# Kernel optimization log

Measured on AMD Instinct MI355X. Metric: run time of the kernel, lower is better.

Reference implementation:

```python
import jax, jax.numpy as jnp
import numpy as np

D_MODEL = 512
N_HEADS = 8
Q_SEQ_LEN = 1024
KV_SEQ_LEN = 1024
N_MODES = 64
D_HEAD = D_MODEL // N_HEADS

# FEDformer frequency_modes (deterministic/lowest branch): lowest n_modes freqs
Q_MODES = np.arange(min(N_MODES, Q_SEQ_LEN // 2))
KV_MODES = np.arange(min(N_MODES, KV_SEQ_LEN // 2))


def setup_inputs() -> dict:
    key = jax.random.key(0)
    kq, kk, kv, kwr, kwi = jax.random.split(key, 5)
    B = 8
    scale = 1.0 / (D_MODEL * D_MODEL)
    return {
        "query": jax.random.normal(kq, (B, N_HEADS, Q_SEQ_LEN, D_HEAD), jnp.float32),
        "key": jax.random.normal(kk, (B, N_HEADS, KV_SEQ_LEN, D_HEAD), jnp.float32),
        "value": jax.random.normal(kv, (B, N_HEADS, KV_SEQ_LEN, D_HEAD), jnp.float32),
        "weights_re": scale * jax.random.uniform(kwr, (N_HEADS, D_HEAD, D_HEAD, len(Q_MODES)), jnp.float32),
        "weights_im": scale * jax.random.uniform(kwi, (N_HEADS, D_HEAD, D_HEAD, len(Q_MODES)), jnp.float32),
    }


def reference(query, key, value, weights_re, weights_im):
    # value is accepted but unused by the original forward (FEA-f variant).
    B, H, L, D = query.shape
    q_modes = jnp.asarray(Q_MODES)
    kv_modes = jnp.asarray(KV_MODES)

    # [B,H,D,L] -> rfft along time -> gather selected frequency modes
    q_fft = jnp.fft.rfft(jnp.swapaxes(query, -2, -1), axis=-1)   # [B,H,D,L//2+1]
    k_fft = jnp.fft.rfft(jnp.swapaxes(key, -2, -1), axis=-1)     # [B,H,D,Lk//2+1]
    q_fft = jnp.take(q_fft, q_modes, axis=-1)                    # [B,H,D,Mq]
    k_fft = jnp.take(k_fft, kv_modes, axis=-1)                   # [B,H,D,Mk]

    # complex attention in frequency domain (no conjugation, as in torch einsum)
    scores_fft = jnp.einsum('bhdq,bhdk->bhqk', q_fft, k_fft)
    attn_fft = jnp.tanh(scores_fft)
    context_fft = jnp.einsum('bhqk,bhdk->bhdq', attn_fft, k_fft)  # [B,H,D,Mq]

    w = (weights_re + 1j * weights_im).astype(jnp.complex64)      # [H,D,D,Mq]
    context_fft = jnp.einsum('bhiq,hijq->bhjq', context_fft, w)   # [B,H,D,Mq]

    # scatter modes back into full rfft spectrum, then irfft
    out_fft = jnp.zeros((B, H, D, L // 2 + 1), jnp.complex64)
    out_fft = out_fft.at[..., q_modes].set(context_fft)
    d_model = H * D
    context = jnp.fft.irfft(out_fft / d_model / d_model, n=L, axis=-1)  # [B,H,D,L]
    return context
```

## Files before the change

### kernel.cpp

```cpp
#include <hip/hip_runtime.h>
#include <hip/hip_bf16.h>
#include <cmath>

#define BATCH 8
#define NH 8
#define BH 64
#define SEQ 1024
#define DH 64
#define NM 64

#define P_PLANE 4096
#define P_FLOATS (2*8*64*2*4096)
#define PR_OFF   P_FLOATS
#define C1C_OFF  (PR_OFF + 2*64*2*4096)
#define C2_OFF   (C1C_OFF + 64*64*64*2)

__global__ __launch_bounds__(256) void k_dft(const float* __restrict__ q,
                                             const float* __restrict__ k,
                                             float* __restrict__ P) {
  const int bid = blockIdx.x;
  const int bh = bid & 63;
  const int inp = (bid >> 6) & 1;
  const int tq = bid >> 7;
  const float* x = (inp ? k : q) + (size_t)bh * (SEQ * DH);

  __shared__ float se[64 * 68], so[64 * 68];
  const int tid = threadIdx.x;
  const int dg = tid & 7;
  const int par = (tid >> 3) & 1;
  const int pg = (tid >> 4) & 1;
  const int mg = tid >> 5;
  const int d0 = dg * 8;

  const int t0g = tq * 64;
  {
    const float4* srcA = reinterpret_cast<const float4*>(x + (size_t)t0g * DH);
    const float4* srcB = reinterpret_cast<const float4*>(x + (size_t)(t0g + 512) * DH);
#pragma unroll
    for (int i = 0; i < 4; ++i) {
      int idx = tid + i * 256;
      int tt = idx >> 4, d4 = (idx & 15) * 4;
      float4 a = srcA[idx], b = srcB[idx];
      *reinterpret_cast<float4*>(&se[tt * 68 + d4]) =
          make_float4(a.x + b.x, a.y + b.y, a.z + b.z, a.w + b.w);
      *reinterpret_cast<float4*>(&so[tt * 68 + d4]) =
          make_float4(a.x - b.x, a.y - b.y, a.z - b.z, a.w - b.w);
    }
  }
  __syncthreads();

  const float* s = pg ? so : se;

  float accr[4][8] = {{0.f}}, acci[4][8] = {{0.f}};
  float stepc[4], steps[4], wr[4], wi[4];
#pragma unroll
  for (int mi = 0; mi < 4; ++mi) {
    const int m = 2 * (mg * 4 + mi) + pg;
    const int ps = (2 * m) & 1023;
    stepc[mi] = cospif((float)ps * (1.0f / 512.0f));
    steps[mi] = -sinpif((float)ps * (1.0f / 512.0f));
    const int p0 = (m * (t0g + par)) & 1023;
    wr[mi] = cospif((float)p0 * (1.0f / 512.0f));
    wi[mi] = -sinpif((float)p0 * (1.0f / 512.0f));
  }

#pragma unroll 4
  for (int k2 = 0; k2 < 32; ++k2) {
    const int tl = 2 * k2 + par;
    float4 a = *reinterpret_cast<const float4*>(&s[tl * 68 + d0]);
    float4 b = *reinterpret_cast<const float4*>(&s[tl * 68 + d0 + 4]);
    float xv[8] = {a.x, a.y, a.z, a.w, b.x, b.y, b.z, b.w};
#pragma unroll
    for (int mi = 0; mi < 4; ++mi) {
      float cwr = wr[mi], cwi = wi[mi];
#pragma unroll
      for (int di = 0; di < 8; ++di) {
        accr[mi][di] = fmaf(cwr, xv[di], accr[mi][di]);
        acci[mi][di] = fmaf(cwi, xv[di], acci[mi][di]);
      }
      float nr = cwr * stepc[mi] - cwi * steps[mi];
      float ni = cwr * steps[mi] + cwi * stepc[mi];
      wr[mi] = nr; wi[mi] = ni;
    }
  }

#pragma unroll
  for (int mi = 0; mi < 4; ++mi) {
#pragma unroll
    for (int di = 0; di < 8; ++di) {
      accr[mi][di] += __shfl_xor(accr[mi][di], 8, 64);
      acci[mi][di] += __shfl_xor(acci[mi][di], 8, 64);
    }
  }

  if (par == 0) {
    const size_t base = (((size_t)inp * 8 + tq) * 64 + bh) * 2 * P_PLANE;
#pragma unroll
    for (int mi = 0; mi < 4; ++mi) {
      const int m = 2 * (mg * 4 + mi) + pg;
      float* pr = P + base + (size_t)m * 64 + d0;
      float* pi = P + base + P_PLANE + (size_t)m * 64 + d0;
      *reinterpret_cast<float4*>(pr) =
          make_float4(accr[mi][0], accr[mi][1], accr[mi][2], accr[mi][3]);
      *reinterpret_cast<float4*>(pr + 4) =
          make_float4(accr[mi][4], accr[mi][5], accr[mi][6], accr[mi][7]);
      *reinterpret_cast<float4*>(pi) =
          make_float4(acci[mi][0], acci[mi][1], acci[mi][2], acci[mi][3]);
      *reinterpret_cast<float4*>(pi + 4) =
          make_float4(acci[mi][4], acci[mi][5], acci[mi][6], acci[mi][7]);
    }
  }
}

__global__ __launch_bounds__(256) void k_red(const float* __restrict__ P,
                                             float* __restrict__ Pr) {
  const int idx = blockIdx.x * 256 + threadIdx.x;
  const int inp = idx >> 17;
  const int r = idx & 131071;
  const float4* p4 = reinterpret_cast<const float4*>(P);
  const size_t base = ((size_t)inp * 8) * 131072 + r;
  float4 acc = p4[base];
#pragma unroll
  for (int t = 1; t < 8; ++t) {
    float4 v = p4[base + (size_t)t * 131072];
    acc.x += v.x; acc.y += v.y; acc.z += v.z; acc.w += v.w;
  }
  reinterpret_cast<float4*>(Pr)[idx] = acc;
}

__device__ __forceinline__ void ctanh_f(float x, float y, float& rr, float& ri) {
  float a = 2.0f * x, b = 2.0f * y;
  if (fabsf(a) > 20.0f) {
    rr = (a > 0.0f) ? 1.0f : -1.0f;
    ri = 0.0f;
  } else {
    float ea = expf(a), ena = expf(-a);
    float sb, cb;
    sincosf(b, &sb, &cb);
    float den = 0.5f * (ea + ena) + cb;
    rr = 0.5f * (ea - ena) / den;
    ri = sb / den;
  }
}

__global__ __launch_bounds__(256) void k_mid_a(const float* __restrict__ Pr,
                                               float* __restrict__ C1c) {
  __shared__ float Kr[64][68], Ki[64][68];
  __shared__ float Qr[8][68], Qi[8][68];
  __shared__ float Ar[8][68], Ai[8][68];
  __shared__ float C1rs[64][9], C1is[64][9];

  const int tid = threadIdx.x;
  const int bh = blockIdx.x >> 3;
  const int qo = blockIdx.x & 7;

  const float4* kbase = reinterpret_cast<const float4*>(Pr + ((size_t)(64 + bh)) * 8192);
  for (int idx = tid; idx < 1024; idx += 256) {
    int kk = idx >> 4, dd = (idx & 15) * 4;
    float4 vr = kbase[idx];
    float4 vi = kbase[idx + 1024];
    *reinterpret_cast<float4*>(&Kr[kk][dd]) = vr;
    *reinterpret_cast<float4*>(&Ki[kk][dd]) = vi;
  }
  {
    const float4* qbase =
        reinterpret_cast<const float4*>(Pr + (size_t)bh * 8192 + (size_t)qo * 8 * 64);
    if (tid < 128) {
      int qi2 = tid >> 4, dd = (tid & 15) * 4;
      float4 vr = qbase[tid];
      float4 vi = qbase[tid + 1024];
      *reinterpret_cast<float4*>(&Qr[qi2][dd]) = vr;
      *reinterpret_cast<float4*>(&Qi[qi2][dd]) = vi;
    }
  }
  __syncthreads();

  {
    const int q = tid >> 5, k0 = tid & 31;
    float sr[2] = {0.f}, si[2] = {0.f};
    for (int d = 0; d < 64; d += 4) {
      const float4 qr = *reinterpret_cast<const float4*>(&Qr[q][d]);
      const float4 qi = *reinterpret_cast<const float4*>(&Qi[q][d]);
#pragma unroll
      for (int j = 0; j < 2; ++j) {
        const int kk = k0 + 32 * j;
        const float4 kr = *reinterpret_cast<const float4*>(&Kr[kk][d]);
        const float4 ki = *reinterpret_cast<const float4*>(&Ki[kk][d]);
        float s0 = sr[j], s1 = si[j];
        s0 = fmaf(qr.x, kr.x, s0); s0 = fmaf(-qi.x, ki.x, s0);
        s1 = fmaf(qr.x, ki.x, s1); s1 = fmaf(qi.x, kr.x, s1);
        s0 = fmaf(qr.y, kr.y, s0); s0 = fmaf(-qi.y, ki.y, s0);
        s1 = fmaf(qr.y, ki.y, s1); s1 = fmaf(qi.y, kr.y, s1);
        s0 = fmaf(qr.z, kr.z, s0); s0 = fmaf(-qi.z, ki.z, s0);
        s1 = fmaf(qr.z, ki.z, s1); s1 = fmaf(qi.z, kr.z, s1);
        s0 = fmaf(qr.w, kr.w, s0); s0 = fmaf(-qi.w, ki.w, s0);
        s1 = fmaf(qr.w, ki.w, s1); s1 = fmaf(qi.w, kr.w, s1);
        sr[j] = s0; si[j] = s1;
      }
    }
#pragma unroll
    for (int j = 0; j < 2; ++j) {
      float rr, ri;
      ctanh_f(sr[j], si[j], rr, ri);
      Ar[q][k0 + 32 * j] = rr;
      Ai[q][k0 + 32 * j] = ri;
    }
  }
  __syncthreads();

  {
    const int q = tid >> 5, d0 = (tid & 31) * 2;
    float cr[2] = {0.f}, ci[2] = {0.f};
    for (int kk = 0; kk < 64; ++kk) {
      float a_r = Ar[q][kk], a_i = Ai[q][kk];
      const float2 kr = *reinterpret_cast<const float2*>(&Kr[kk][d0]);
      const float2 ki = *reinterpret_cast<const float2*>(&Ki[kk][d0]);
      cr[0] = fmaf(a_r, kr.x, cr[0]); cr[0] = fmaf(-a_i, ki.x, cr[0]);
      ci[0] = fmaf(a_r, ki.x, ci[0]); ci[0] = fmaf(a_i, kr.x, ci[0]);
      cr[1] = fmaf(a_r, kr.y, cr[1]); cr[1] = fmaf(-a_i, ki.y, cr[1]);
      ci[1] = fmaf(a_r, ki.y, ci[1]); ci[1] = fmaf(a_i, kr.y, ci[1]);
    }
    C1rs[d0][q] = cr[0];     C1is[d0][q] = ci[0];
    C1rs[d0 + 1][q] = cr[1]; C1is[d0 + 1][q] = ci[1];
  }
  __syncthreads();

  for (int idx = tid; idx < 512; idx += 256) {
    int i = idx >> 3, ql = idx & 7;
    size_t o = (((size_t)bh * 64 + i) * 64 + qo * 8 + ql) * 2;
    *reinterpret_cast<float2*>(&C1c[o]) = make_float2(C1rs[i][ql], C1is[i][ql]);
  }
}

__global__ __launch_bounds__(64) void k_mid_b(const float* __restrict__ C1c,
                                              const float* __restrict__ wre,
                                              const float* __restrict__ wim,
                                              float* __restrict__ C2) {
  const int bid = blockIdx.x;
  const int j = bid & 63;
  const int h = (bid >> 6) & 7;
  const int bq = bid >> 9;
  const int lane = threadIdx.x;

  const int bh0 = (bq * 2 + 0) * 8 + h;
  const int bh1 = (bq * 2 + 1) * 8 + h;
  const float2* c1a = reinterpret_cast<const float2*>(C1c) + (size_t)bh0 * 4096 + lane;
  const float2* c1b = reinterpret_cast<const float2*>(C1c) + (size_t)bh1 * 4096 + lane;
  const float* wrp = wre + ((size_t)h * 4096 + j) * 64 + lane;
  const float* wip = wim + ((size_t)h * 4096 + j) * 64 + lane;

  float ar0 = 0.f, ai0 = 0.f, ar1 = 0.f, ai1 = 0.f;
#pragma unroll 8
  for (int i = 0; i < 64; ++i) {
    float wr = wrp[(size_t)i * 4096];
    float wi = wip[(size_t)i * 4096];
    float2 ca = c1a[(size_t)i * 64];
    float2 cb = c1b[(size_t)i * 64];
    ar0 = fmaf(ca.x, wr, ar0); ar0 = fmaf(-ca.y, wi, ar0);
    ai0 = fmaf(ca.x, wi, ai0); ai0 = fmaf(ca.y, wr, ai0);
    ar1 = fmaf(cb.x, wr, ar1); ar1 = fmaf(-cb.y, wi, ar1);
    ai1 = fmaf(cb.x, wi, ai1); ai1 = fmaf(cb.y, wr, ai1);
  }
  *reinterpret_cast<float2*>(&C2[(((size_t)bh0 * 64 + j) * 64 + lane) * 2]) = make_float2(ar0, ai0);
  *reinterpret_cast<float2*>(&C2[(((size_t)bh1 * 64 + j) * 64 + lane) * 2]) = make_float2(ar1, ai1);
}

__global__ __launch_bounds__(256) void k_idft(const float* __restrict__ C2,
                                              float* __restrict__ out) {
  __shared__ float Cr[64][68], Ci[64][68];
  const int tid = threadIdx.x;
  const int bh = blockIdx.x >> 3;
  const int tc = blockIdx.x & 7;
  const float s = 1.0f / (512.0f * 512.0f * 1024.0f);

  for (int idx = tid; idx < 4096; idx += 256) {
    int j = idx >> 6, m = idx & 63;
    float f = (m == 0) ? s : 2.0f * s;
    float2 c = *reinterpret_cast<const float2*>(&C2[(((size_t)bh * 64 + j) * 64 + m) * 2]);
    Cr[m][j] = f * c.x;
    Ci[m][j] = f * c.y;
  }
  __syncthreads();

  const int tg = tid & 31, jg = tid >> 5;
  const int tp0 = tc * 64 + tg * 2;
  const int j0 = jg * 8;

  float sc[2], ss[2], wc[2], wsn[2];
#pragma unroll
  for (int kk = 0; kk < 2; ++kk) {
    float ph = (float)((tp0 + kk) & 1023) * (1.0f / 512.0f);
    sc[kk] = cospif(ph);
    ss[kk] = sinpif(ph);
    wc[kk] = 1.0f;
    wsn[kk] = 0.0f;
  }

  float accE[2][8] = {{0.f}}, accO[2][8] = {{0.f}};
#pragma unroll 2
  for (int m = 0; m < 64; ++m) {
    float4 c0 = *reinterpret_cast<const float4*>(&Cr[m][j0]);
    float4 c1 = *reinterpret_cast<const float4*>(&Cr[m][j0 + 4]);
    float4 e0 = *reinterpret_cast<const float4*>(&Ci[m][j0]);
    float4 e1 = *reinterpret_cast<const float4*>(&Ci[m][j0 + 4]);
    float crv[8] = {c0.x, c0.y, c0.z, c0.w, c1.x, c1.y, c1.z, c1.w};
    float civ[8] = {e0.x, e0.y, e0.z, e0.w, e1.x, e1.y, e1.z, e1.w};
    float(*acc)[8] = (m & 1) ? accO : accE;
#pragma unroll
    for (int kk = 0; kk < 2; ++kk) {
      float cw = wc[kk], sw = wsn[kk];
#pragma unroll
      for (int jj = 0; jj < 8; ++jj) {
        acc[kk][jj] = fmaf(crv[jj], cw, acc[kk][jj]);
        acc[kk][jj] = fmaf(-civ[jj], sw, acc[kk][jj]);
      }
      float nr = cw * sc[kk] - sw * ss[kk];
      float ni = cw * ss[kk] + sw * sc[kk];
      wc[kk] = nr; wsn[kk] = ni;
    }
  }

#pragma unroll
  for (int jj = 0; jj < 8; ++jj) {
    float e0v = accE[0][jj], o0v = accO[0][jj];
    float e1v = accE[1][jj], o1v = accO[1][jj];
    float* row = &out[((size_t)bh * 64 + j0 + jj) * 1024];
    *reinterpret_cast<float2*>(&row[tp0])       = make_float2(e0v + o0v, e1v + o1v);
    *reinterpret_cast<float2*>(&row[tp0 + 512]) = make_float2(e0v - o0v, e1v - o1v);
  }
}

extern "C" void kernel_launch(void* const* d_in, const int* in_sizes, int n_in,
                              void* d_out, int out_size, void* d_ws, size_t ws_size,
                              hipStream_t stream) {
  const float* q   = (const float*)d_in[0];
  const float* k   = (const float*)d_in[1];
  const float* wre = (const float*)d_in[3];
  const float* wim = (const float*)d_in[4];
  float* out = (float*)d_out;
  float* ws  = (float*)d_ws;

  float* P   = ws;
  float* Pr  = ws + PR_OFF;
  float* C1c = ws + C1C_OFF;
  float* C2  = ws + C2_OFF;

  k_dft  <<<1024, 256, 0, stream>>>(q, k, P);
  k_red  <<<1024, 256, 0, stream>>>(P, Pr);
  k_mid_a<<<512,  256, 0, stream>>>(Pr, C1c);
  k_mid_b<<<2048,  64, 0, stream>>>(C1c, wre, wim, C2);
  k_idft <<<512,  256, 0, stream>>>(C2, out);
}
```

Before: 166.6 us.

## Rebalance work per thread across mid and inverse-DFT kernels for more parallelism

```diff
diff --git a/kernel.cpp b/kernel.cpp
--- a/kernel.cpp
+++ b/kernel.cpp
@@ -146,13 +146,13 @@
 __global__ __launch_bounds__(256) void k_mid_a(const float* __restrict__ Pr,
                                                float* __restrict__ C1c) {
   __shared__ float Kr[64][68], Ki[64][68];
-  __shared__ float Qr[8][68], Qi[8][68];
-  __shared__ float Ar[8][68], Ai[8][68];
-  __shared__ float C1rs[64][9], C1is[64][9];
+  __shared__ float Qr[4][68], Qi[4][68];
+  __shared__ float Ar[4][68], Ai[4][68];
+  __shared__ float C1rs[64][6], C1is[64][6];
 
   const int tid = threadIdx.x;
-  const int bh = blockIdx.x >> 3;
-  const int qo = blockIdx.x & 7;
+  const int bh = blockIdx.x >> 4;
+  const int qo = blockIdx.x & 15;
 
   const float4* kbase = reinterpret_cast<const float4*>(Pr + ((size_t)(64 + bh)) * 8192);
   for (int idx = tid; idx < 1024; idx += 256) {
@@ -164,8 +164,8 @@
   }
   {
     const float4* qbase =
-        reinterpret_cast<const float4*>(Pr + (size_t)bh * 8192 + (size_t)qo * 8 * 64);
-    if (tid < 128) {
+        reinterpret_cast<const float4*>(Pr + (size_t)bh * 8192 + (size_t)qo * 256);
+    if (tid < 64) {
       int qi2 = tid >> 4, dd = (tid & 15) * 4;
       float4 vr = qbase[tid];
       float4 vi = qbase[tid + 1024];
@@ -176,58 +176,47 @@
   __syncthreads();
 
   {
-    const int q = tid >> 5, k0 = tid & 31;
-    float sr[2] = {0.f}, si[2] = {0.f};
+    const int q = tid >> 6, kk = tid & 63;
+    float s0 = 0.f, s1 = 0.f;
     for (int d = 0; d < 64; d += 4) {
       const float4 qr = *reinterpret_cast<const float4*>(&Qr[q][d]);
       const float4 qi = *reinterpret_cast<const float4*>(&Qi[q][d]);
-#pragma unroll
-      for (int j = 0; j < 2; ++j) {
-        const int kk = k0 + 32 * j;
-        const float4 kr = *reinterpret_cast<const float4*>(&Kr[kk][d]);
-        const float4 ki = *reinterpret_cast<const float4*>(&Ki[kk][d]);
-        float s0 = sr[j], s1 = si[j];
-        s0 = fmaf(qr.x, kr.x, s0); s0 = fmaf(-qi.x, ki.x, s0);
-        s1 = fmaf(qr.x, ki.x, s1); s1 = fmaf(qi.x, kr.x, s1);
-        s0 = fmaf(qr.y, kr.y, s0); s0 = fmaf(-qi.y, ki.y, s0);
-        s1 = fmaf(qr.y, ki.y, s1); s1 = fmaf(qi.y, kr.y, s1);
-        s0 = fmaf(qr.z, kr.z, s0); s0 = fmaf(-qi.z, ki.z, s0);
-        s1 = fmaf(qr.z, ki.z, s1); s1 = fmaf(qi.z, kr.z, s1);
-        s0 = fmaf(qr.w, kr.w, s0); s0 = fmaf(-qi.w, ki.w, s0);
-        s1 = fmaf(qr.w, ki.w, s1); s1 = fmaf(qi.w, kr.w, s1);
-        sr[j] = s0; si[j] = s1;
-      }
-    }
-#pragma unroll
-    for (int j = 0; j < 2; ++j) {
-      float rr, ri;
-      ctanh_f(sr[j], si[j], rr, ri);
-      Ar[q][k0 + 32 * j] = rr;
-      Ai[q][k0 + 32 * j] = ri;
-    }
-  }
-  __syncthreads();
-
-  {
-    const int q = tid >> 5, d0 = (tid & 31) * 2;
-    float cr[2] = {0.f}, ci[2] = {0.f};
+      const float4 kr = *reinterpret_cast<const float4*>(&Kr[kk][d]);
+      const float4 ki = *reinterpret_cast<const float4*>(&Ki[kk][d]);
+      s0 = fmaf(qr.x, kr.x, s0); s0 = fmaf(-qi.x, ki.x, s0);
+      s1 = fmaf(qr.x, ki.x, s1); s1 = fmaf(qi.x, kr.x, s1);
+      s0 = fmaf(qr.y, kr.y, s0); s0 = fmaf(-qi.y, ki.y, s0);
+      s1 = fmaf(qr.y, ki.y, s1); s1 = fmaf(qi.y, kr.y, s1);
+      s0 = fmaf(qr.z, kr.z, s0); s0 = fmaf(-qi.z, ki.z, s0);
+      s1 = fmaf(qr.z, ki.z, s1); s1 = fmaf(qi.z, kr.z, s1);
+      s0 = fmaf(qr.w, kr.w, s0); s0 = fmaf(-qi.w, ki.w, s0);
+      s1 = fmaf(qr.w, ki.w, s1); s1 = fmaf(qi.w, kr.w, s1);
+    }
+    float rr, ri;
+    ctanh_f(s0, s1, rr, ri);
+    Ar[q][kk] = rr;
+    Ai[q][kk] = ri;
+  }
+  __syncthreads();
+
+  {
+    const int q = tid >> 6, dd = tid & 63;
+    float cr = 0.f, ci = 0.f;
+#pragma unroll 8
     for (int kk = 0; kk < 64; ++kk) {
       float a_r = Ar[q][kk], a_i = Ai[q][kk];
-      const float2 kr = *reinterpret_cast<const float2*>(&Kr[kk][d0]);
-      const float2 ki = *reinterpret_cast<const float2*>(&Ki[kk][d0]);
-      cr[0] = fmaf(a_r, kr.x, cr[0]); cr[0] = fmaf(-a_i, ki.x, cr[0]);
-      ci[0] = fmaf(a_r, ki.x, ci[0]); ci[0] = fmaf(a_i, kr.x, ci[0]);
-      cr[1] = fmaf(a_r, kr.y, cr[1]); cr[1] = fmaf(-a_i, ki.y, cr[1]);
-      ci[1] = fmaf(a_r, ki.y, ci[1]); ci[1] = fmaf(a_i, kr.y, ci[1]);
-    }
-    C1rs[d0][q] = cr[0];     C1is[d0][q] = ci[0];
-    C1rs[d0 + 1][q] = cr[1]; C1is[d0 + 1][q] = ci[1];
-  }
-  __syncthreads();
-
-  for (int idx = tid; idx < 512; idx += 256) {
-    int i = idx >> 3, ql = idx & 7;
-    size_t o = (((size_t)bh * 64 + i) * 64 + qo * 8 + ql) * 2;
+      float krv = Kr[kk][dd], kiv = Ki[kk][dd];
+      cr = fmaf(a_r, krv, cr); cr = fmaf(-a_i, kiv, cr);
+      ci = fmaf(a_r, kiv, ci); ci = fmaf(a_i, krv, ci);
+    }
+    C1rs[dd][q] = cr;
+    C1is[dd][q] = ci;
+  }
+  __syncthreads();
+
+  {
+    const int i = tid >> 2, ql = tid & 3;
+    size_t o = (((size_t)bh * 64 + i) * 64 + qo * 4 + ql) * 2;
     *reinterpret_cast<float2*>(&C1c[o]) = make_float2(C1rs[i][ql], C1is[i][ql]);
   }
 }
@@ -239,30 +228,25 @@
   const int bid = blockIdx.x;
   const int j = bid & 63;
   const int h = (bid >> 6) & 7;
-  const int bq = bid >> 9;
+  const int b = bid >> 9;
   const int lane = threadIdx.x;
 
-  const int bh0 = (bq * 2 + 0) * 8 + h;
-  const int bh1 = (bq * 2 + 1) * 8 + h;
-  const float2* c1a = reinterpret_cast<const float2*>(C1c) + (size_t)bh0 * 4096 + lane;
-  const float2* c1b = reinterpret_cast<const float2*>(C1c) + (size_t)bh1 * 4096 + lane;
+  const int bh = b * 8 + h;
+  const float2* c1 = reinterpret_cast<const float2*>(C1c) + (size_t)bh * 4096 + lane;
   const float* wrp = wre + ((size_t)h * 4096 + j) * 64 + lane;
   const float* wip = wim + ((size_t)h * 4096 + j) * 64 + lane;
 
-  float ar0 = 0.f, ai0 = 0.f, ar1 = 0.f, ai1 = 0.f;
+  float ar = 0.f, ai = 0.f;
 #pragma unroll 8
   for (int i = 0; i < 64; ++i) {
     float wr = wrp[(size_t)i * 4096];
     float wi = wip[(size_t)i * 4096];
-    float2 ca = c1a[(size_t)i * 64];
-    float2 cb = c1b[(size_t)i * 64];
-    ar0 = fmaf(ca.x, wr, ar0); ar0 = fmaf(-ca.y, wi, ar0);
-    ai0 = fmaf(ca.x, wi, ai0); ai0 = fmaf(ca.y, wr, ai0);
-    ar1 = fmaf(cb.x, wr, ar1); ar1 = fmaf(-cb.y, wi, ar1);
-    ai1 = fmaf(cb.x, wi, ai1); ai1 = fmaf(cb.y, wr, ai1);
-  }
-  *reinterpret_cast<float2*>(&C2[(((size_t)bh0 * 64 + j) * 64 + lane) * 2]) = make_float2(ar0, ai0);
-  *reinterpret_cast<float2*>(&C2[(((size_t)bh1 * 64 + j) * 64 + lane) * 2]) = make_float2(ar1, ai1);
+    float2 c = c1[(size_t)i * 64];
+    ar = fmaf(c.x, wr, ar); ar = fmaf(-c.y, wi, ar);
+    ai = fmaf(c.x, wi, ai); ai = fmaf(c.y, wr, ai);
+  }
+  *reinterpret_cast<float2*>(&C2[(((size_t)bh * 64 + j) * 64 + lane) * 2]) =
+      make_float2(ar, ai);
 }
 
 __global__ __launch_bounds__(256) void k_idft(const float* __restrict__ C2,
@@ -282,13 +266,13 @@
   }
   __syncthreads();
 
-  const int tg = tid & 31, jg = tid >> 5;
-  const int tp0 = tc * 64 + tg * 2;
-  const int j0 = jg * 8;
-
-  float sc[2], ss[2], wc[2], wsn[2];
-#pragma unroll
-  for (int kk = 0; kk < 2; ++kk) {
+  const int tg = tid & 15, jg = tid >> 4;
+  const int tp0 = tc * 64 + tg * 4;
+  const int j0 = jg * 4;
+
+  float sc[4], ss[4], wc[4], wsn[4];
+#pragma unroll
+  for (int kk = 0; kk < 4; ++kk) {
     float ph = (float)((tp0 + kk) & 1023) * (1.0f / 512.0f);
     sc[kk] = cospif(ph);
     ss[kk] = sinpif(ph);
@@ -296,21 +280,19 @@
     wsn[kk] = 0.0f;
   }
 
-  float accE[2][8] = {{0.f}}, accO[2][8] = {{0.f}};
+  float accE[4][4] = {{0.f}}, accO[4][4] = {{0.f}};
 #pragma unroll 2
   for (int m = 0; m < 64; ++m) {
     float4 c0 = *reinterpret_cast<const float4*>(&Cr[m][j0]);
-    float4 c1 = *reinterpret_cast<const float4*>(&Cr[m][j0 + 4]);
     float4 e0 = *reinterpret_cast<const float4*>(&Ci[m][j0]);
-    float4 e1 = *reinterpret_cast<const float4*>(&Ci[m][j0 + 4]);
-    float crv[8] = {c0.x, c0.y, c0.z, c0.w, c1.x, c1.y, c1.z, c1.w};
-    float civ[8] = {e0.x, e0.y, e0.z, e0.w, e1.x, e1.y, e1.z, e1.w};
-    float(*acc)[8] = (m & 1) ? accO : accE;
-#pragma unroll
-    for (int kk = 0; kk < 2; ++kk) {
+    float crv[4] = {c0.x, c0.y, c0.z, c0.w};
+    float civ[4] = {e0.x, e0.y, e0.z, e0.w};
+    float(*acc)[4] = (m & 1) ? accO : accE;
+#pragma unroll
+    for (int kk = 0; kk < 4; ++kk) {
       float cw = wc[kk], sw = wsn[kk];
 #pragma unroll
-      for (int jj = 0; jj < 8; ++jj) {
+      for (int jj = 0; jj < 4; ++jj) {
         acc[kk][jj] = fmaf(crv[jj], cw, acc[kk][jj]);
         acc[kk][jj] = fmaf(-civ[jj], sw, acc[kk][jj]);
       }
@@ -321,12 +303,14 @@
   }
 
 #pragma unroll
-  for (int jj = 0; jj < 8; ++jj) {
-    float e0v = accE[0][jj], o0v = accO[0][jj];
-    float e1v = accE[1][jj], o1v = accO[1][jj];
+  for (int jj = 0; jj < 4; ++jj) {
     float* row = &out[((size_t)bh * 64 + j0 + jj) * 1024];
-    *reinterpret_cast<float2*>(&row[tp0])       = make_float2(e0v + o0v, e1v + o1v);
-    *reinterpret_cast<float2*>(&row[tp0 + 512]) = make_float2(e0v - o0v, e1v - o1v);
+    *reinterpret_cast<float4*>(&row[tp0]) =
+        make_float4(accE[0][jj] + accO[0][jj], accE[1][jj] + accO[1][jj],
+                    accE[2][jj] + accO[2][jj], accE[3][jj] + accO[3][jj]);
+    *reinterpret_cast<float4*>(&row[tp0 + 512]) =
+        make_float4(accE[0][jj] - accO[0][jj], accE[1][jj] - accO[1][jj],
+                    accE[2][jj] - accO[2][jj], accE[3][jj] - accO[3][jj]);
   }
 }
 
@@ -347,7 +331,7 @@
 
   k_dft  <<<1024, 256, 0, stream>>>(q, k, P);
   k_red  <<<1024, 256, 0, stream>>>(P, Pr);
-  k_mid_a<<<512,  256, 0, stream>>>(Pr, C1c);
-  k_mid_b<<<2048,  64, 0, stream>>>(C1c, wre, wim, C2);
+  k_mid_a<<<1024, 256, 0, stream>>>(Pr, C1c);
+  k_mid_b<<<4096,  64, 0, stream>>>(C1c, wre, wim, C2);
   k_idft <<<512,  256, 0, stream>>>(C2, out);
 }
```

New measurement: 170.2 us. +2.2%, slower.
